# Kernel tuning notes

Measured on AMD Instinct MI355X. Metric: run time of the kernel, lower is better.

## Reference

```python
import jax, jax.numpy as jnp
import numpy as np

D_MODEL = 1024
BLOCK_SIZE = 2048


def setup_inputs() -> dict:
    key = jax.random.key(0)
    ks = jax.random.split(key, 9)
    B, T, C = 4, 2048, D_MODEL
    s = 1.0 / np.sqrt(C)
    return {
        "x": jax.random.normal(ks[0], (B, T, C), dtype=jnp.float32),
        "Wq": jax.random.normal(ks[1], (C, C), dtype=jnp.float32) * s,
        "bq": jnp.zeros((C,), dtype=jnp.float32),
        "Wk": jax.random.normal(ks[2], (C, C), dtype=jnp.float32) * s,
        "bk": jnp.zeros((C,), dtype=jnp.float32),
        "Wv": jax.random.normal(ks[3], (C, C), dtype=jnp.float32) * s,
        "bv": jnp.zeros((C,), dtype=jnp.float32),
        "Wo": jax.random.normal(ks[4], (C, C), dtype=jnp.float32) * s,
        "bo": jnp.zeros((C,), dtype=jnp.float32),
    }


def reference(x, Wq, bq, Wk, bk, Wv, bv, Wo, bo):
    B, T, C = x.shape
    q = x @ Wq + bq
    k = x @ Wk + bk
    v = x @ Wv + bv
    # NOTE: original module never splits heads; attention is over full d_model
    score = jnp.einsum("btc,bsc->bts", q, k) / jnp.sqrt(jnp.asarray(C, x.dtype))
    causal = jnp.tril(jnp.ones((T, T), dtype=bool))
    score = jnp.where(causal, score, jnp.asarray(-jnp.inf, x.dtype))
    probs = jax.nn.softmax(score, axis=-1)
    out = jnp.einsum("bts,bsc->btc", probs, v)
    return out @ Wo + bo
```

## Files before the change

### kernel.cpp

```cpp
#include <hip/hip_runtime.h>
#include <hip/hip_bf16.h>
#include <stdint.h>


typedef __attribute__((ext_vector_type(8))) __bf16 bf16x8;
typedef __attribute__((ext_vector_type(4))) float f32x4;

#define MFMA16(A, B, C) __builtin_amdgcn_mfma_f32_16x16x32_bf16(A, B, C, 0, 0, 0)
#define BAR() asm volatile("s_barrier" ::: "memory")

#define T_SEQ 2048
#define D_MOD 1024

static __device__ __forceinline__ void gload_lds16(const void* g, void* l) {
  __builtin_amdgcn_global_load_lds(
      (const __attribute__((address_space(1))) void*)g,
      (__attribute__((address_space(3))) void*)l, 16, 0, 0);
}

__global__ void cvt_bf16_kernel(const float* __restrict__ in,
                                __bf16* __restrict__ out, int n8) {
  int i = blockIdx.x * blockDim.x + threadIdx.x;
  if (i < n8) {
    const float4* p = (const float4*)(in + (size_t)i * 8);
    float4 a = p[0], b = p[1];
    bf16x8 o;
    o[0] = (__bf16)a.x; o[1] = (__bf16)a.y; o[2] = (__bf16)a.z; o[3] = (__bf16)a.w;
    o[4] = (__bf16)b.x; o[5] = (__bf16)b.y; o[6] = (__bf16)b.z; o[7] = (__bf16)b.w;
    *(bf16x8*)(out + (size_t)i * 8) = o;
  }
}

__global__ void transpose_cvt_kernel(const float* __restrict__ W,
                                     __bf16* __restrict__ Wt) {
  __shared__ float tile[32][33];
  int tx = threadIdx.x, ty = threadIdx.y;
  int bx = blockIdx.x * 32, by = blockIdx.y * 32;
#pragma unroll
  for (int i = 0; i < 4; i++)
    tile[ty + 8 * i][tx] = W[(size_t)(by + ty + 8 * i) * D_MOD + bx + tx];
  __syncthreads();
#pragma unroll
  for (int i = 0; i < 4; i++)
    Wt[(size_t)(bx + ty + 8 * i) * D_MOD + by + tx] = (__bf16)tile[tx][ty + 8 * i];
}

__global__ void transpose_v_kernel(const __bf16* __restrict__ V,
                                   __bf16* __restrict__ Vt) {
  __shared__ __bf16 tile[32][33];
  int tx = threadIdx.x, ty = threadIdx.y;
  int b = blockIdx.z;
  int t0 = blockIdx.x * 32, d0 = blockIdx.y * 32;
  const __bf16* Vb = V + (size_t)b * T_SEQ * D_MOD;
  __bf16* Vtb = Vt + (size_t)b * D_MOD * T_SEQ;
#pragma unroll
  for (int i = 0; i < 4; i++)
    tile[ty + 8 * i][tx] = Vb[(size_t)(t0 + ty + 8 * i) * D_MOD + d0 + tx];
  __syncthreads();
#pragma unroll
  for (int i = 0; i < 4; i++)
    Vtb[(size_t)(d0 + ty + 8 * i) * T_SEQ + t0 + tx] = tile[tx][ty + 8 * i];
}

template <int MG, int NG>
static __device__ __forceinline__ void mfma_quad(f32x4 (&acc)[8][4],
                                                 const bf16x8 (&aR)[4][2],
                                                 const bf16x8 (&bR)[2][2]) {
#pragma unroll
  for (int i = 0; i < 4; i++)
#pragma unroll
    for (int n = 0; n < 2; n++)
#pragma unroll
      for (int kk = 0; kk < 2; kk++)
        acc[MG * 4 + i][NG * 2 + n] =
            MFMA16(aR[i][kk], bR[n][kk], acc[MG * 4 + i][NG * 2 + n]);
}

template <int MODE>
__global__ __launch_bounds__(512, 2) void gemm8_kernel(
    const __bf16* __restrict__ A, const __bf16* __restrict__ Bt,
    const float* __restrict__ b0, const float* __restrict__ b1,
    const float* __restrict__ b2, void* __restrict__ o0,
    void* __restrict__ o1, void* __restrict__ o2, int lda, int ldb,
    size_t bsA, size_t bsB, size_t bsC) {
  constexpr int NT = 16;
  __shared__ __align__(16) char lds[131072];
#define ABUF(p, h) (lds + ((p) * 2 + (h)) * 16384)
#define BBUF(p, h) (lds + 65536 + ((p) * 2 + (h)) * 16384)

  const int tid = threadIdx.x;
  const int w = tid >> 6, l = tid & 63;
  const int wr = w >> 2, wc = w & 3;
  int bm, bn;
  if (MODE == 0) {
    const int cpx = gridDim.x >> 3;
    const int swz = ((int)blockIdx.x & 7) * cpx + ((int)blockIdx.x >> 3);
    bm = (swz / 12) * 256;
    bn = (swz % 12) * 256;
  } else {
    if ((int)blockIdx.y > (int)blockIdx.x) return;
    bm = blockIdx.x * 256;
    bn = blockIdx.y * 256;
  }
  const int z = blockIdx.z;
  A += (size_t)z * bsA;
  Bt += (size_t)z * bsB;

  const int grow = l >> 2;
  const int cswz = (l & 3) ^ ((l >> 3) & 3);
  const int rlo = l & 15;
  const int xsw = (((l >> 4) ^ ((l >> 1) & 3)) << 4);

#define STAGE_A(t, h)                                                        \
  {                                                                          \
    const __bf16* g = A + (size_t)(bm + (h) * 128 + w * 16 + grow) * lda +   \
                      (t) * 64 + cswz * 8;                                   \
    char* d = ABUF((t) & 1, h) + w * 1024 + l * 16;                          \
    gload_lds16(g, d);                                                       \
    gload_lds16(g + 32, d + 8192);                                           \
  }
#define STAGE_B(t, h)                                                        \
  {                                                                          \
    const __bf16* g = Bt + (size_t)(bn + (h) * 128 + w * 16 + grow) * ldb +  \
                      (t) * 64 + cswz * 8;                                   \
    char* d = BBUF((t) & 1, h) + w * 1024 + l * 16;                          \
    gload_lds16(g, d);                                                       \
    gload_lds16(g + 32, d + 8192);                                           \
  }
#define LDA_FRAG(p, g, i, kk)                                     \
  (*(const bf16x8*)(ABUF(p, wr) + (kk) * 8192 +                   \
                    ((g) * 64 + (i) * 16 + rlo) * 64 + xsw))
#define LDB_FRAG(p, g, n, kk)                                     \
  (*(const bf16x8*)(BBUF(p, (wc >> 1)) + (kk) * 8192 +            \
                    ((wc & 1) * 64 + (g) * 32 + (n) * 16 + rlo) * 64 + xsw))

  f32x4 acc[8][4] = {};
  STAGE_A(0, 0); STAGE_A(0, 1);
  STAGE_B(0, 0); STAGE_B(0, 1);
  STAGE_A(1, 0); STAGE_A(1, 1);
  asm volatile("s_waitcnt vmcnt(4)" ::: "memory");
  BAR();

  for (int t = 0; t < NT; ++t) {
    const int p = t & 1;
    bf16x8 a[4][2], b[2][2];
#pragma unroll
    for (int i = 0; i < 4; i++) {
      a[i][0] = LDA_FRAG(p, 0, i, 0);
      a[i][1] = LDA_FRAG(p, 0, i, 1);
    }
#pragma unroll
    for (int n = 0; n < 2; n++) {
      b[n][0] = LDB_FRAG(p, 0, n, 0);
      b[n][1] = LDB_FRAG(p, 0, n, 1);
    }
    if (t + 1 < NT) STAGE_B(t + 1, 0);
    BAR();
    __builtin_amdgcn_s_setprio(1);
    mfma_quad<0, 0>(acc, a, b);
    __builtin_amdgcn_s_setprio(0);
    BAR();
    bf16x8 b2[2][2];
#pragma unroll
    for (int n = 0; n < 2; n++) {
      b2[n][0] = LDB_FRAG(p, 1, n, 0);
      b2[n][1] = LDB_FRAG(p, 1, n, 1);
    }
    if (t + 1 < NT) STAGE_B(t + 1, 1);
    BAR();
    __builtin_amdgcn_s_setprio(1);
    mfma_quad<0, 1>(acc, a, b2);
    __builtin_amdgcn_s_setprio(0);
    BAR();
#pragma unroll
    for (int i = 0; i < 4; i++) {
      a[i][0] = LDA_FRAG(p, 1, i, 0);
      a[i][1] = LDA_FRAG(p, 1, i, 1);
    }
    BAR();
    __builtin_amdgcn_s_setprio(1);
    mfma_quad<1, 1>(acc, a, b2);
    __builtin_amdgcn_s_setprio(0);
    BAR();
#pragma unroll
    for (int n = 0; n < 2; n++) {
      b[n][0] = LDB_FRAG(p, 0, n, 0);
      b[n][1] = LDB_FRAG(p, 0, n, 1);
    }
    if (t + 2 < NT) {
      STAGE_A(t + 2, 0); STAGE_A(t + 2, 1);
      BAR();
      __builtin_amdgcn_s_setprio(1);
      mfma_quad<1, 0>(acc, a, b);
      __builtin_amdgcn_s_setprio(0);
      asm volatile("s_waitcnt vmcnt(4)" ::: "memory");
      BAR();
    } else {
      BAR();
      __builtin_amdgcn_s_setprio(1);
      mfma_quad<1, 0>(acc, a, b);
      __builtin_amdgcn_s_setprio(0);
      asm volatile("s_waitcnt vmcnt(0)" ::: "memory");
      BAR();
    }
  }

  if (MODE == 0) {
    const int seg = bn >> 10;
    const float* bs = (seg == 0) ? b0 : (seg == 1) ? b1 : b2;
    __bf16* os = (__bf16*)((seg == 0) ? o0 : (seg == 1) ? o1 : o2);
    const int bnl = bn & 1023;
#pragma unroll
    for (int n4 = 0; n4 < 4; n4++) {
      int col = bnl + wc * 64 + n4 * 16 + rlo;
      float bvv = bs[col];
#pragma unroll
      for (int mi = 0; mi < 8; mi++) {
        int row = bm + wr * 128 + mi * 16 + (l >> 4) * 4;
#pragma unroll
        for (int r = 0; r < 4; r++)
          os[(size_t)(row + r) * D_MOD + col] = (__bf16)(acc[mi][n4][r] + bvv);
      }
    }
  } else {
    float* os = (float*)o0 + (size_t)z * bsC;
#pragma unroll
    for (int n4 = 0; n4 < 4; n4++) {
      int col = bn + wc * 64 + n4 * 16 + rlo;
#pragma unroll
      for (int mi = 0; mi < 8; mi++) {
        int rowb = bm + wr * 128 + mi * 16 + (l >> 4) * 4;
#pragma unroll
        for (int r = 0; r < 4; r++) {
          int row = rowb + r;
          float v = acc[mi][n4][r] * 0.03125f;
          if (col > row) v = -1e30f;
          os[(size_t)row * T_SEQ + col] = v;
        }
      }
    }
  }
#undef ABUF
#undef BBUF
#undef STAGE_A
#undef STAGE_B
#undef LDA_FRAG
#undef LDB_FRAG
}

template <int MODE>
__global__ __launch_bounds__(512, 2) void ugemm_kernel(
    const __bf16* __restrict__ A, const __bf16* __restrict__ Bt,
    const float* __restrict__ b0, void* __restrict__ o0, int lda, int ldb,
    size_t bsA, size_t bsB, size_t bsC) {
  __shared__ __align__(16) char lds[147456];
#define ABUF(p3) (lds + (p3) * 16384)
#define BBUF(p3) (lds + 49152 + (p3) * 32768)

  const int tid = threadIdx.x;
  const int w = tid >> 6, l = tid & 63;
  const int wr = w >> 2, wc = w & 3;
  const int z = blockIdx.z;

  int bm, bn, NT;
  if (MODE == 1) {
    const int cpx = gridDim.x >> 3;
    const int swz = ((int)blockIdx.x & 7) * cpx + ((int)blockIdx.x >> 3);
    bm = (swz >> 2) * 128; bn = (swz & 3) * 256; NT = 16;
  } else {
    const int i = (int)blockIdx.x >> 2;
    bm = i * 128; bn = ((int)blockIdx.x & 3) * 256; NT = (i + 1) * 2;
  }
  A += (size_t)z * bsA;
  Bt += (size_t)z * bsB;

  const int grow = w * 16 + (l >> 2);
  const int cswz = (l & 3) ^ ((l >> 3) & 3);
  const int rlo = l & 15;
  const int xsw = (((l >> 4) ^ ((l >> 1) & 3)) << 4);

#define STAGE_A(t, p3)                                                       \
  {                                                                          \
    const __bf16* g = A + (size_t)(bm + grow) * lda + (t) * 64 + cswz * 8;   \
    char* d = ABUF(p3) + w * 1024 + l * 16;                                  \
    gload_lds16(g, d);                                                       \
    gload_lds16(g + 32, d + 8192);                                           \
  }
#define STAGE_B(t, p3)                                                       \
  {                                                                          \
    const __bf16* g = Bt + (size_t)(bn + grow) * ldb + (t) * 64 + cswz * 8;  \
    char* d = BBUF(p3) + w * 1024 + l * 16;                                  \
    gload_lds16(g, d);                                                       \
    gload_lds16(g + 32, d + 16384);                                          \
    const __bf16* g2 = g + (size_t)128 * ldb;                                \
    gload_lds16(g2, d + 8192);                                               \
    gload_lds16(g2 + 32, d + 8192 + 16384);                                  \
  }
#define LDA_FRAG(p3, i, kk)                                       \
  (*(const bf16x8*)(ABUF(p3) + (kk) * 8192 +                      \
                    (wr * 64 + (i) * 16 + rlo) * 64 + xsw))
#define LDB_FRAG(p3, n, kk)                                       \
  (*(const bf16x8*)(BBUF(p3) + (kk) * 16384 +                     \
                    (wc * 64 + (n) * 16 + rlo) * 64 + xsw))

  f32x4 acc[4][4] = {};
  STAGE_A(0, 0); STAGE_B(0, 0);
  STAGE_A(1, 1); STAGE_B(1, 1);
  asm volatile("s_waitcnt vmcnt(6)" ::: "memory");
  BAR();

  int p = 0, pn2 = 2;
  for (int t = 0; t < NT; ++t) {
    bf16x8 af[4][2], bf01[2][2], bf23[2][2];
#pragma unroll
    for (int i = 0; i < 4; i++) {
      af[i][0] = LDA_FRAG(p, i, 0);
      af[i][1] = LDA_FRAG(p, i, 1);
    }
#pragma unroll
    for (int n = 0; n < 2; n++) {
      bf01[n][0] = LDB_FRAG(p, n, 0);
      bf01[n][1] = LDB_FRAG(p, n, 1);
    }
    if (t + 2 < NT) STAGE_A(t + 2, pn2);
    BAR();
    __builtin_amdgcn_s_setprio(1);
#pragma unroll
    for (int i = 0; i < 4; i++)
#pragma unroll
      for (int n = 0; n < 2; n++) {
        acc[i][n] = MFMA16(af[i][0], bf01[n][0], acc[i][n]);
        acc[i][n] = MFMA16(af[i][1], bf01[n][1], acc[i][n]);
      }
    __builtin_amdgcn_s_setprio(0);
    BAR();
#pragma unroll
    for (int n = 0; n < 2; n++) {
      bf23[n][0] = LDB_FRAG(p, n + 2, 0);
      bf23[n][1] = LDB_FRAG(p, n + 2, 1);
    }
    if (t + 2 < NT) STAGE_B(t + 2, pn2);
    BAR();
    __builtin_amdgcn_s_setprio(1);
#pragma unroll
    for (int i = 0; i < 4; i++)
#pragma unroll
      for (int n = 0; n < 2; n++) {
        acc[i][n + 2] = MFMA16(af[i][0], bf23[n][0], acc[i][n + 2]);
        acc[i][n + 2] = MFMA16(af[i][1], bf23[n][1], acc[i][n + 2]);
      }
    __builtin_amdgcn_s_setprio(0);
    if (t + 2 < NT) {
      asm volatile("s_waitcnt vmcnt(6)" ::: "memory");
    } else {
      asm volatile("s_waitcnt vmcnt(0)" ::: "memory");
    }
    BAR();
    p = (p + 1 == 3) ? 0 : p + 1;
    pn2 = (pn2 + 1 == 3) ? 0 : pn2 + 1;
  }

  if (MODE == 1) {
    float* os = (float*)o0;
#pragma unroll
    for (int n = 0; n < 4; n++) {
      int col = bn + wc * 64 + n * 16 + rlo;
      float bvv = b0[col];
#pragma unroll
      for (int m = 0; m < 4; m++) {
        int rowb = bm + wr * 64 + m * 16 + (l >> 4) * 4;
#pragma unroll
        for (int r = 0; r < 4; r++)
          os[(size_t)(rowb + r) * D_MOD + col] = acc[m][n][r] + bvv;
      }
    }
  } else {
    __bf16* os = (__bf16*)o0 + (size_t)z * bsC;
#pragma unroll
    for (int n = 0; n < 4; n++) {
      int col = bn + wc * 64 + n * 16 + rlo;
#pragma unroll
      for (int m = 0; m < 4; m++) {
        int rowb = bm + wr * 64 + m * 16 + (l >> 4) * 4;
#pragma unroll
        for (int r = 0; r < 4; r++)
          os[(size_t)(rowb + r) * D_MOD + col] = (__bf16)acc[m][n][r];
      }
    }
  }
#undef ABUF
#undef BBUF
#undef STAGE_A
#undef STAGE_B
#undef LDA_FRAG
#undef LDB_FRAG
}

__global__ __launch_bounds__(256) void softmax_kernel(float* __restrict__ S,
                                                      size_t bstride) {
  const int t = blockIdx.x, b = blockIdx.y;
  float* Srow = S + (size_t)b * bstride + (size_t)t * T_SEQ;
  __bf16* Prow = (__bf16*)Srow;
  const int L = ((t + 1) + 127) & ~127;
  const int tid = threadIdx.x;
  const int base = tid * 8;
  const bool act = base < L;
  float v[8];
  float m = -1e30f;
  if (act) {
    float4 a = *(const float4*)(Srow + base);
    float4 c = *(const float4*)(Srow + base + 4);
    v[0] = a.x; v[1] = a.y; v[2] = a.z; v[3] = a.w;
    v[4] = c.x; v[5] = c.y; v[6] = c.z; v[7] = c.w;
#pragma unroll
    for (int j = 0; j < 8; j++) m = fmaxf(m, v[j]);
  }
#pragma unroll
  for (int off = 1; off < 64; off <<= 1) m = fmaxf(m, __shfl_xor(m, off));
  __shared__ float redm[4], reds[4];
  const int wave = tid >> 6, lane = tid & 63;
  if (lane == 0) redm[wave] = m;
  __syncthreads();
  m = fmaxf(fmaxf(redm[0], redm[1]), fmaxf(redm[2], redm[3]));
  float p[8];
  float s = 0.f;
  if (act) {
#pragma unroll
    for (int j = 0; j < 8; j++) {
      p[j] = __expf(v[j] - m);
      s += p[j];
    }
  }
#pragma unroll
  for (int off = 1; off < 64; off <<= 1) s += __shfl_xor(s, off);
  if (lane == 0) reds[wave] = s;
  __syncthreads();
  const float inv = 1.0f / (reds[0] + reds[1] + reds[2] + reds[3]);
  if (act) {
    bf16x8 o;
#pragma unroll
    for (int j = 0; j < 8; j++) o[j] = (__bf16)(p[j] * inv);
    *(bf16x8*)(Prow + base) = o;
  }
}

extern "C" void kernel_launch(void* const* d_in, const int* in_sizes, int n_in,
                              void* d_out, int out_size, void* d_ws,
                              size_t ws_size, hipStream_t stream) {
  const float* x = (const float*)d_in[0];
  const float* Wq = (const float*)d_in[1];
  const float* bq = (const float*)d_in[2];
  const float* Wk = (const float*)d_in[3];
  const float* bk = (const float*)d_in[4];
  const float* Wv = (const float*)d_in[5];
  const float* bv = (const float*)d_in[6];
  const float* Wo = (const float*)d_in[7];
  const float* bo = (const float*)d_in[8];

  char* ws = (char*)d_ws;
  const size_t MB = 1u << 20;
  const size_t TC = (size_t)T_SEQ * D_MOD;
  const size_t TT = (size_t)T_SEQ * T_SEQ;
  __bf16* xb    = (__bf16*)(ws);
  __bf16* Wqkvt = (__bf16*)(ws + 16 * MB);
  __bf16* Wot   = (__bf16*)(ws + 22 * MB);
  __bf16* Qb    = (__bf16*)(ws + 24 * MB);
  __bf16* Kb    = (__bf16*)(ws + 40 * MB);
  __bf16* Vb    = (__bf16*)(ws + 56 * MB);
  __bf16* Vtb   = (__bf16*)(ws);

  cvt_bf16_kernel<<<4096, 256, 0, stream>>>(x, xb, 8192 * D_MOD / 8);
  dim3 tb(32, 8);
  transpose_cvt_kernel<<<dim3(32, 32), tb, 0, stream>>>(Wq, Wqkvt);
  transpose_cvt_kernel<<<dim3(32, 32), tb, 0, stream>>>(Wk, Wqkvt + 1024 * 1024);
  transpose_cvt_kernel<<<dim3(32, 32), tb, 0, stream>>>(Wv, Wqkvt + 2048 * 1024);
  transpose_cvt_kernel<<<dim3(32, 32), tb, 0, stream>>>(Wo, Wot);
  gemm8_kernel<0><<<384, 512, 0, stream>>>(xb, Wqkvt, bq, bk, bv, Qb, Kb, Vb,
                                           D_MOD, D_MOD, 0, 0, 0);
  transpose_v_kernel<<<dim3(64, 32, 4), tb, 0, stream>>>(Vb, Vtb);

  const bool batched = ws_size >= 137 * MB;
  if (batched) {
    float* S = (float*)(ws + 72 * MB);
    __bf16* AO = Vb;
    gemm8_kernel<3><<<dim3(8, 8, 4), 512, 0, stream>>>(
        Qb, Kb, nullptr, nullptr, nullptr, S, nullptr, nullptr, D_MOD, D_MOD,
        TC, TC, TT);
    softmax_kernel<<<dim3(T_SEQ, 4), 256, 0, stream>>>(S, TT);
    ugemm_kernel<2><<<dim3(64, 1, 4), 512, 0, stream>>>(
        (const __bf16*)S, Vtb, nullptr, AO, 2 * T_SEQ, T_SEQ, TT * 2,
        (size_t)D_MOD * T_SEQ, TC);
    ugemm_kernel<1><<<256, 512, 0, stream>>>(AO, Wot, bo, d_out, D_MOD, D_MOD,
                                             0, 0, 0);
  } else {
    float* S = (float*)(ws + 56 * MB);
    __bf16* AO = Qb;
    for (int b = 0; b < 4; ++b) {
      gemm8_kernel<3><<<dim3(8, 8, 1), 512, 0, stream>>>(
          Qb + b * TC, Kb + b * TC, nullptr, nullptr, nullptr, S, nullptr,
          nullptr, D_MOD, D_MOD, 0, 0, 0);
      softmax_kernel<<<dim3(T_SEQ, 1), 256, 0, stream>>>(S, 0);
      ugemm_kernel<2><<<dim3(64, 1, 1), 512, 0, stream>>>(
          (const __bf16*)S, Vtb + b * TC, nullptr, AO + b * TC, 2 * T_SEQ,
          T_SEQ, 0, 0, 0);
    }
    ugemm_kernel<1><<<256, 512, 0, stream>>>(AO, Wot, bo, d_out, D_MOD, D_MOD,
                                             0, 0, 0);
  }
}
```

Before: 197.4 us.

## Fuse V transpose into QKV epilogue, merge weight transposes, rebalance causal PV tiles

The QKV GEMM epilogue now writes V directly transposed, which removes the separate transpose_v kernel. The four weight transposes become one launch. The 256x256 GEMM mainloop is simplified to a single-buffered 64KB-LDS loop. The PV GEMM uses 128x128 tiles, and each block processes a short and a long causal row block together to balance work. Risks: the single-buffered GEMM may expose load latency, and the transposed V stores are strided 8-byte writes.

```diff
diff --git a/kernel.cpp b/kernel.cpp
--- a/kernel.cpp
+++ b/kernel.cpp
@@ -4,6 +4,7 @@
 
 
 typedef __attribute__((ext_vector_type(8))) __bf16 bf16x8;
+typedef __attribute__((ext_vector_type(4))) __bf16 bf16x4;
 typedef __attribute__((ext_vector_type(4))) float f32x4;
 
 #define MFMA16(A, B, C) __builtin_amdgcn_mfma_f32_16x16x32_bf16(A, B, C, 0, 0, 0)
@@ -31,9 +32,16 @@
   }
 }
 
-__global__ void transpose_cvt_kernel(const float* __restrict__ W,
-                                     __bf16* __restrict__ Wt) {
+__global__ void transpose_cvt4_kernel(const float* __restrict__ Wq,
+                                      const float* __restrict__ Wk,
+                                      const float* __restrict__ Wv,
+                                      const float* __restrict__ Wo,
+                                      __bf16* __restrict__ Wqkvt,
+                                      __bf16* __restrict__ Wot) {
   __shared__ float tile[32][33];
+  const int z = blockIdx.z;
+  const float* W = (z == 0) ? Wq : (z == 1) ? Wk : (z == 2) ? Wv : Wo;
+  __bf16* Wt = (z < 3) ? (Wqkvt + (size_t)z * 1024 * 1024) : Wot;
   int tx = threadIdx.x, ty = threadIdx.y;
   int bx = blockIdx.x * 32, by = blockIdx.y * 32;
 #pragma unroll
@@ -45,48 +53,17 @@
     Wt[(size_t)(bx + ty + 8 * i) * D_MOD + by + tx] = (__bf16)tile[tx][ty + 8 * i];
 }
 
-__global__ void transpose_v_kernel(const __bf16* __restrict__ V,
-                                   __bf16* __restrict__ Vt) {
-  __shared__ __bf16 tile[32][33];
-  int tx = threadIdx.x, ty = threadIdx.y;
-  int b = blockIdx.z;
-  int t0 = blockIdx.x * 32, d0 = blockIdx.y * 32;
-  const __bf16* Vb = V + (size_t)b * T_SEQ * D_MOD;
-  __bf16* Vtb = Vt + (size_t)b * D_MOD * T_SEQ;
-#pragma unroll
-  for (int i = 0; i < 4; i++)
-    tile[ty + 8 * i][tx] = Vb[(size_t)(t0 + ty + 8 * i) * D_MOD + d0 + tx];
-  __syncthreads();
-#pragma unroll
-  for (int i = 0; i < 4; i++)
-    Vtb[(size_t)(d0 + ty + 8 * i) * T_SEQ + t0 + tx] = tile[tx][ty + 8 * i];
-}
-
-template <int MG, int NG>
-static __device__ __forceinline__ void mfma_quad(f32x4 (&acc)[8][4],
-                                                 const bf16x8 (&aR)[4][2],
-                                                 const bf16x8 (&bR)[2][2]) {
-#pragma unroll
-  for (int i = 0; i < 4; i++)
-#pragma unroll
-    for (int n = 0; n < 2; n++)
-#pragma unroll
-      for (int kk = 0; kk < 2; kk++)
-        acc[MG * 4 + i][NG * 2 + n] =
-            MFMA16(aR[i][kk], bR[n][kk], acc[MG * 4 + i][NG * 2 + n]);
-}
-
 template <int MODE>
-__global__ __launch_bounds__(512, 2) void gemm8_kernel(
+__global__ __launch_bounds__(512, 2) void sbg_kernel(
     const __bf16* __restrict__ A, const __bf16* __restrict__ Bt,
-    const float* __restrict__ b0, const float* __restrict__ b1,
-    const float* __restrict__ b2, void* __restrict__ o0,
-    void* __restrict__ o1, void* __restrict__ o2, int lda, int ldb,
-    size_t bsA, size_t bsB, size_t bsC) {
+    const float* __restrict__ bq, const float* __restrict__ bk,
+    const float* __restrict__ bv, void* __restrict__ o0,
+    void* __restrict__ o1, void* __restrict__ o2, size_t bsA, size_t bsB,
+    size_t bsC) {
   constexpr int NT = 16;
-  __shared__ __align__(16) char lds[131072];
-#define ABUF(p, h) (lds + ((p) * 2 + (h)) * 16384)
-#define BBUF(p, h) (lds + 65536 + ((p) * 2 + (h)) * 16384)
+  __shared__ __align__(16) char lds[65536];
+  char* ABUF = lds;
+  char* BBUF = lds + 32768;
 
   const int tid = threadIdx.x;
   const int w = tid >> 6, l = tid & 63;
@@ -103,123 +80,101 @@
     bn = blockIdx.y * 256;
   }
   const int z = blockIdx.z;
-  A += (size_t)z * bsA;
-  Bt += (size_t)z * bsB;
-
-  const int grow = l >> 2;
+  const __bf16* Ag = A + (size_t)z * bsA + (size_t)bm * 1024;
+  const __bf16* Bg = Bt + (size_t)z * bsB + (size_t)bn * 1024;
+
   const int cswz = (l & 3) ^ ((l >> 3) & 3);
   const int rlo = l & 15;
   const int xsw = (((l >> 4) ^ ((l >> 1) & 3)) << 4);
-
-#define STAGE_A(t, h)                                                        \
-  {                                                                          \
-    const __bf16* g = A + (size_t)(bm + (h) * 128 + w * 16 + grow) * lda +   \
-                      (t) * 64 + cswz * 8;                                   \
-    char* d = ABUF((t) & 1, h) + w * 1024 + l * 16;                          \
-    gload_lds16(g, d);                                                       \
-    gload_lds16(g + 32, d + 8192);                                           \
-  }
-#define STAGE_B(t, h)                                                        \
-  {                                                                          \
-    const __bf16* g = Bt + (size_t)(bn + (h) * 128 + w * 16 + grow) * ldb +  \
-                      (t) * 64 + cswz * 8;                                   \
-    char* d = BBUF((t) & 1, h) + w * 1024 + l * 16;                          \
-    gload_lds16(g, d);                                                       \
-    gload_lds16(g + 32, d + 8192);                                           \
-  }
-#define LDA_FRAG(p, g, i, kk)                                     \
-  (*(const bf16x8*)(ABUF(p, wr) + (kk) * 8192 +                   \
-                    ((g) * 64 + (i) * 16 + rlo) * 64 + xsw))
-#define LDB_FRAG(p, g, n, kk)                                     \
-  (*(const bf16x8*)(BBUF(p, (wc >> 1)) + (kk) * 8192 +            \
-                    ((wc & 1) * 64 + (g) * 32 + (n) * 16 + rlo) * 64 + xsw))
+  const int srow = w * 16 + (l >> 2);
+
+#define SSTAGE(dst, gsrc, t)                                              \
+  {                                                                       \
+    _Pragma("unroll") for (int h = 0; h < 2; h++) {                       \
+      const __bf16* g =                                                   \
+          (gsrc) + (size_t)(h * 128 + srow) * 1024 + (t) * 64 + cswz * 8; \
+      char* d = (dst) + h * 8192 + w * 1024 + l * 16;                     \
+      gload_lds16(g, d);                                                  \
+      gload_lds16(g + 32, d + 16384);                                     \
+    }                                                                     \
+  }
 
   f32x4 acc[8][4] = {};
-  STAGE_A(0, 0); STAGE_A(0, 1);
-  STAGE_B(0, 0); STAGE_B(0, 1);
-  STAGE_A(1, 0); STAGE_A(1, 1);
-  asm volatile("s_waitcnt vmcnt(4)" ::: "memory");
+  SSTAGE(ABUF, Ag, 0);
+  SSTAGE(BBUF, Bg, 0);
+  asm volatile("s_waitcnt vmcnt(0)" ::: "memory");
   BAR();
 
   for (int t = 0; t < NT; ++t) {
-    const int p = t & 1;
-    bf16x8 a[4][2], b[2][2];
-#pragma unroll
-    for (int i = 0; i < 4; i++) {
-      a[i][0] = LDA_FRAG(p, 0, i, 0);
-      a[i][1] = LDA_FRAG(p, 0, i, 1);
-    }
-#pragma unroll
-    for (int n = 0; n < 2; n++) {
-      b[n][0] = LDB_FRAG(p, 0, n, 0);
-      b[n][1] = LDB_FRAG(p, 0, n, 1);
-    }
-    if (t + 1 < NT) STAGE_B(t + 1, 0);
-    BAR();
+    bf16x8 af[8][2], bf[4][2];
+#pragma unroll
+    for (int i = 0; i < 8; i++) {
+#pragma unroll
+      for (int kk = 0; kk < 2; kk++)
+        af[i][kk] = *(const bf16x8*)(ABUF + kk * 16384 +
+                                     (wr * 128 + i * 16 + rlo) * 64 + xsw);
+    }
+#pragma unroll
+    for (int n = 0; n < 4; n++) {
+#pragma unroll
+      for (int kk = 0; kk < 2; kk++)
+        bf[n][kk] = *(const bf16x8*)(BBUF + kk * 16384 +
+                                     (wc * 64 + n * 16 + rlo) * 64 + xsw);
+    }
+    asm volatile("s_waitcnt lgkmcnt(0)" ::: "memory");
+    BAR();
+    if (t + 1 < NT) {
+      SSTAGE(ABUF, Ag, t + 1);
+      SSTAGE(BBUF, Bg, t + 1);
+    }
     __builtin_amdgcn_s_setprio(1);
-    mfma_quad<0, 0>(acc, a, b);
+#pragma unroll
+    for (int kk = 0; kk < 2; kk++)
+#pragma unroll
+      for (int i = 0; i < 8; i++)
+#pragma unroll
+        for (int n = 0; n < 4; n++)
+          acc[i][n] = MFMA16(af[i][kk], bf[n][kk], acc[i][n]);
     __builtin_amdgcn_s_setprio(0);
-    BAR();
-    bf16x8 b2[2][2];
-#pragma unroll
-    for (int n = 0; n < 2; n++) {
-      b2[n][0] = LDB_FRAG(p, 1, n, 0);
-      b2[n][1] = LDB_FRAG(p, 1, n, 1);
-    }
-    if (t + 1 < NT) STAGE_B(t + 1, 1);
-    BAR();
-    __builtin_amdgcn_s_setprio(1);
-    mfma_quad<0, 1>(acc, a, b2);
-    __builtin_amdgcn_s_setprio(0);
-    BAR();
-#pragma unroll
-    for (int i = 0; i < 4; i++) {
-      a[i][0] = LDA_FRAG(p, 1, i, 0);
-      a[i][1] = LDA_FRAG(p, 1, i, 1);
-    }
-    BAR();
-    __builtin_amdgcn_s_setprio(1);
-    mfma_quad<1, 1>(acc, a, b2);
-    __builtin_amdgcn_s_setprio(0);
-    BAR();
-#pragma unroll
-    for (int n = 0; n < 2; n++) {
-      b[n][0] = LDB_FRAG(p, 0, n, 0);
-      b[n][1] = LDB_FRAG(p, 0, n, 1);
-    }
-    if (t + 2 < NT) {
-      STAGE_A(t + 2, 0); STAGE_A(t + 2, 1);
-      BAR();
-      __builtin_amdgcn_s_setprio(1);
-      mfma_quad<1, 0>(acc, a, b);
-      __builtin_amdgcn_s_setprio(0);
-      asm volatile("s_waitcnt vmcnt(4)" ::: "memory");
-      BAR();
-    } else {
-      BAR();
-      __builtin_amdgcn_s_setprio(1);
-      mfma_quad<1, 0>(acc, a, b);
-      __builtin_amdgcn_s_setprio(0);
-      asm volatile("s_waitcnt vmcnt(0)" ::: "memory");
-      BAR();
-    }
-  }
-
+    asm volatile("s_waitcnt vmcnt(0)" ::: "memory");
+    BAR();
+  }
+
+  const int l4 = (l >> 4) * 4;
   if (MODE == 0) {
     const int seg = bn >> 10;
-    const float* bs = (seg == 0) ? b0 : (seg == 1) ? b1 : b2;
-    __bf16* os = (__bf16*)((seg == 0) ? o0 : (seg == 1) ? o1 : o2);
     const int bnl = bn & 1023;
-#pragma unroll
-    for (int n4 = 0; n4 < 4; n4++) {
-      int col = bnl + wc * 64 + n4 * 16 + rlo;
-      float bvv = bs[col];
-#pragma unroll
-      for (int mi = 0; mi < 8; mi++) {
-        int row = bm + wr * 128 + mi * 16 + (l >> 4) * 4;
-#pragma unroll
-        for (int r = 0; r < 4; r++)
-          os[(size_t)(row + r) * D_MOD + col] = (__bf16)(acc[mi][n4][r] + bvv);
+    if (seg < 2) {
+      const float* bs = seg ? bk : bq;
+      __bf16* os = (__bf16*)(seg ? o1 : o0);
+#pragma unroll
+      for (int n4 = 0; n4 < 4; n4++) {
+        int col = bnl + wc * 64 + n4 * 16 + rlo;
+        float bvv = bs[col];
+#pragma unroll
+        for (int mi = 0; mi < 8; mi++) {
+          int row = bm + wr * 128 + mi * 16 + l4;
+#pragma unroll
+          for (int r = 0; r < 4; r++)
+            os[(size_t)(row + r) * D_MOD + col] = (__bf16)(acc[mi][n4][r] + bvv);
+        }
+      }
+    } else {
+      __bf16* os = (__bf16*)o2;
+#pragma unroll
+      for (int n4 = 0; n4 < 4; n4++) {
+        int lcol = bnl + wc * 64 + n4 * 16 + rlo;
+        float bvv = bv[lcol];
+#pragma unroll
+        for (int mi = 0; mi < 8; mi++) {
+          int rowb = bm + wr * 128 + mi * 16 + l4;
+          int zz = rowb >> 11, tt = rowb & 2047;
+          bf16x4 pk;
+#pragma unroll
+          for (int r = 0; r < 4; r++) pk[r] = (__bf16)(acc[mi][n4][r] + bvv);
+          *(bf16x4*)(os + (size_t)zz * (D_MOD * T_SEQ) + (size_t)lcol * T_SEQ +
+                     tt) = pk;
+        }
       }
     }
   } else {
@@ -229,7 +184,7 @@
       int col = bn + wc * 64 + n4 * 16 + rlo;
 #pragma unroll
       for (int mi = 0; mi < 8; mi++) {
-        int rowb = bm + wr * 128 + mi * 16 + (l >> 4) * 4;
+        int rowb = bm + wr * 128 + mi * 16 + l4;
 #pragma unroll
         for (int r = 0; r < 4; r++) {
           int row = rowb + r;
@@ -240,59 +195,150 @@
       }
     }
   }
-#undef ABUF
-#undef BBUF
-#undef STAGE_A
-#undef STAGE_B
-#undef LDA_FRAG
-#undef LDB_FRAG
-}
-
-template <int MODE>
-__global__ __launch_bounds__(512, 2) void ugemm_kernel(
-    const __bf16* __restrict__ A, const __bf16* __restrict__ Bt,
-    const float* __restrict__ b0, void* __restrict__ o0, int lda, int ldb,
-    size_t bsA, size_t bsB, size_t bsC) {
-  __shared__ __align__(16) char lds[147456];
+#undef SSTAGE
+}
+
+__global__ __launch_bounds__(512, 2) void pv_kernel(
+    const __bf16* __restrict__ Ap, const __bf16* __restrict__ Btp,
+    __bf16* __restrict__ Op, size_t bsA, size_t bsB, size_t bsC) {
+  __shared__ __align__(16) char lds[98304];
 #define ABUF(p3) (lds + (p3) * 16384)
-#define BBUF(p3) (lds + 49152 + (p3) * 32768)
+#define BBUF(p3) (lds + 49152 + (p3) * 16384)
 
   const int tid = threadIdx.x;
   const int w = tid >> 6, l = tid & 63;
   const int wr = w >> 2, wc = w & 3;
+  const int pid = (int)blockIdx.x >> 3;
+  const int bn = ((int)blockIdx.x & 7) * 128;
   const int z = blockIdx.z;
-
-  int bm, bn, NT;
-  if (MODE == 1) {
-    const int cpx = gridDim.x >> 3;
-    const int swz = ((int)blockIdx.x & 7) * cpx + ((int)blockIdx.x >> 3);
-    bm = (swz >> 2) * 128; bn = (swz & 3) * 256; NT = 16;
-  } else {
-    const int i = (int)blockIdx.x >> 2;
-    bm = i * 128; bn = ((int)blockIdx.x & 3) * 256; NT = (i + 1) * 2;
-  }
-  A += (size_t)z * bsA;
-  Bt += (size_t)z * bsB;
+  const __bf16* A = Ap + (size_t)z * bsA;
+  const __bf16* Bt = Btp + (size_t)z * bsB;
+  __bf16* O = Op + (size_t)z * bsC;
 
   const int grow = w * 16 + (l >> 2);
   const int cswz = (l & 3) ^ ((l >> 3) & 3);
   const int rlo = l & 15;
   const int xsw = (((l >> 4) ^ ((l >> 1) & 3)) << 4);
 
-#define STAGE_A(t, p3)                                                       \
+#define PSTAGE_A(t, p3)                                                      \
   {                                                                          \
-    const __bf16* g = A + (size_t)(bm + grow) * lda + (t) * 64 + cswz * 8;   \
+    const __bf16* g = A + (size_t)(bm + grow) * 4096 + (t) * 64 + cswz * 8;  \
     char* d = ABUF(p3) + w * 1024 + l * 16;                                  \
     gload_lds16(g, d);                                                       \
     gload_lds16(g + 32, d + 8192);                                           \
   }
+#define PSTAGE_B(t, p3)                                                      \
+  {                                                                          \
+    const __bf16* g = Bt + (size_t)(bn + grow) * 2048 + (t) * 64 + cswz * 8; \
+    char* d = BBUF(p3) + w * 1024 + l * 16;                                  \
+    gload_lds16(g, d);                                                       \
+    gload_lds16(g + 32, d + 8192);                                           \
+  }
+#define PLDA(p3, i, kk)                                           \
+  (*(const bf16x8*)(ABUF(p3) + (kk) * 8192 +                      \
+                    (wr * 64 + (i) * 16 + rlo) * 64 + xsw))
+#define PLDB(p3, n, kk)                                           \
+  (*(const bf16x8*)(BBUF(p3) + (kk) * 8192 +                      \
+                    (wc * 32 + (n) * 16 + rlo) * 64 + xsw))
+
+#pragma unroll
+  for (int seg = 0; seg < 2; ++seg) {
+    const int i = seg ? (15 - pid) : pid;
+    const int bm = i * 128;
+    const int NT = (i + 1) * 2;
+    f32x4 acc[4][2] = {};
+
+    PSTAGE_A(0, 0); PSTAGE_B(0, 0);
+    if (NT > 1) { PSTAGE_A(1, 1); PSTAGE_B(1, 1); }
+    asm volatile("s_waitcnt vmcnt(4)" ::: "memory");
+    BAR();
+
+    int p = 0, pn2 = 2;
+    for (int t = 0; t < NT; ++t) {
+      bf16x8 af[4][2], bfv[2][2];
+#pragma unroll
+      for (int m = 0; m < 4; m++) {
+        af[m][0] = PLDA(p, m, 0);
+        af[m][1] = PLDA(p, m, 1);
+      }
+#pragma unroll
+      for (int n = 0; n < 2; n++) {
+        bfv[n][0] = PLDB(p, n, 0);
+        bfv[n][1] = PLDB(p, n, 1);
+      }
+      if (t + 2 < NT) { PSTAGE_A(t + 2, pn2); PSTAGE_B(t + 2, pn2); }
+      BAR();
+      __builtin_amdgcn_s_setprio(1);
+#pragma unroll
+      for (int m = 0; m < 4; m++)
+#pragma unroll
+        for (int n = 0; n < 2; n++) {
+          acc[m][n] = MFMA16(af[m][0], bfv[n][0], acc[m][n]);
+          acc[m][n] = MFMA16(af[m][1], bfv[n][1], acc[m][n]);
+        }
+      __builtin_amdgcn_s_setprio(0);
+      if (t + 2 < NT) asm volatile("s_waitcnt vmcnt(4)" ::: "memory");
+      else asm volatile("s_waitcnt vmcnt(0)" ::: "memory");
+      BAR();
+      p = (p + 1 == 3) ? 0 : p + 1;
+      pn2 = (pn2 + 1 == 3) ? 0 : pn2 + 1;
+    }
+
+#pragma unroll
+    for (int n = 0; n < 2; n++) {
+      int col = bn + wc * 32 + n * 16 + rlo;
+#pragma unroll
+      for (int m = 0; m < 4; m++) {
+        int rowb = bm + wr * 64 + m * 16 + (l >> 4) * 4;
+#pragma unroll
+        for (int r = 0; r < 4; r++)
+          O[(size_t)(rowb + r) * D_MOD + col] = (__bf16)acc[m][n][r];
+      }
+    }
+    BAR();
+  }
+#undef ABUF
+#undef BBUF
+#undef PSTAGE_A
+#undef PSTAGE_B
+#undef PLDA
+#undef PLDB
+}
+
+__global__ __launch_bounds__(512, 2) void oproj_kernel(
+    const __bf16* __restrict__ A, const __bf16* __restrict__ Bt,
+    const float* __restrict__ b0, float* __restrict__ o0) {
+  constexpr int NT = 16;
+  __shared__ __align__(16) char lds[147456];
+#define ABUF(p3) (lds + (p3) * 16384)
+#define BBUF(p3) (lds + 49152 + (p3) * 32768)
+
+  const int tid = threadIdx.x;
+  const int w = tid >> 6, l = tid & 63;
+  const int wr = w >> 2, wc = w & 3;
+  const int cpx = gridDim.x >> 3;
+  const int swz = ((int)blockIdx.x & 7) * cpx + ((int)blockIdx.x >> 3);
+  const int bm = (swz >> 2) * 128, bn = (swz & 3) * 256;
+
+  const int grow = w * 16 + (l >> 2);
+  const int cswz = (l & 3) ^ ((l >> 3) & 3);
+  const int rlo = l & 15;
+  const int xsw = (((l >> 4) ^ ((l >> 1) & 3)) << 4);
+
+#define STAGE_A(t, p3)                                                       \
+  {                                                                          \
+    const __bf16* g = A + (size_t)(bm + grow) * 1024 + (t) * 64 + cswz * 8;  \
+    char* d = ABUF(p3) + w * 1024 + l * 16;                                  \
+    gload_lds16(g, d);                                                       \
+    gload_lds16(g + 32, d + 8192);                                           \
+  }
 #define STAGE_B(t, p3)                                                       \
   {                                                                          \
-    const __bf16* g = Bt + (size_t)(bn + grow) * ldb + (t) * 64 + cswz * 8;  \
+    const __bf16* g = Bt + (size_t)(bn + grow) * 1024 + (t) * 64 + cswz * 8; \
     char* d = BBUF(p3) + w * 1024 + l * 16;                                  \
     gload_lds16(g, d);                                                       \
     gload_lds16(g + 32, d + 16384);                                          \
-    const __bf16* g2 = g + (size_t)128 * ldb;                                \
+    const __bf16* g2 = g + (size_t)128 * 1024;                               \
     gload_lds16(g2, d + 8192);                                               \
     gload_lds16(g2 + 32, d + 8192 + 16384);                                  \
   }
@@ -360,32 +406,16 @@
     pn2 = (pn2 + 1 == 3) ? 0 : pn2 + 1;
   }
 
-  if (MODE == 1) {
-    float* os = (float*)o0;
-#pragma unroll
-    for (int n = 0; n < 4; n++) {
-      int col = bn + wc * 64 + n * 16 + rlo;
-      float bvv = b0[col];
-#pragma unroll
-      for (int m = 0; m < 4; m++) {
-        int rowb = bm + wr * 64 + m * 16 + (l >> 4) * 4;
-#pragma unroll
-        for (int r = 0; r < 4; r++)
-          os[(size_t)(rowb + r) * D_MOD + col] = acc[m][n][r] + bvv;
-      }
-    }
-  } else {
-    __bf16* os = (__bf16*)o0 + (size_t)z * bsC;
-#pragma unroll
-    for (int n = 0; n < 4; n++) {
-      int col = bn + wc * 64 + n * 16 + rlo;
-#pragma unroll
-      for (int m = 0; m < 4; m++) {
-        int rowb = bm + wr * 64 + m * 16 + (l >> 4) * 4;
-#pragma unroll
-        for (int r = 0; r < 4; r++)
-          os[(size_t)(rowb + r) * D_MOD + col] = (__bf16)acc[m][n][r];
-      }
+#pragma unroll
+  for (int n = 0; n < 4; n++) {
+    int col = bn + wc * 64 + n * 16 + rlo;
+    float bvv = b0[col];
+#pragma unroll
+    for (int m = 0; m < 4; m++) {
+      int rowb = bm + wr * 64 + m * 16 + (l >> 4) * 4;
+#pragma unroll
+      for (int r = 0; r < 4; r++)
+        o0[(size_t)(rowb + r) * D_MOD + col] = acc[m][n][r] + bvv;
     }
   }
 #undef ABUF
@@ -466,45 +496,35 @@
   __bf16* Wot   = (__bf16*)(ws + 22 * MB);
   __bf16* Qb    = (__bf16*)(ws + 24 * MB);
   __bf16* Kb    = (__bf16*)(ws + 40 * MB);
-  __bf16* Vb    = (__bf16*)(ws + 56 * MB);
-  __bf16* Vtb   = (__bf16*)(ws);
+  __bf16* Vtb   = (__bf16*)(ws + 56 * MB);
 
   cvt_bf16_kernel<<<4096, 256, 0, stream>>>(x, xb, 8192 * D_MOD / 8);
-  dim3 tb(32, 8);
-  transpose_cvt_kernel<<<dim3(32, 32), tb, 0, stream>>>(Wq, Wqkvt);
-  transpose_cvt_kernel<<<dim3(32, 32), tb, 0, stream>>>(Wk, Wqkvt + 1024 * 1024);
-  transpose_cvt_kernel<<<dim3(32, 32), tb, 0, stream>>>(Wv, Wqkvt + 2048 * 1024);
-  transpose_cvt_kernel<<<dim3(32, 32), tb, 0, stream>>>(Wo, Wot);
-  gemm8_kernel<0><<<384, 512, 0, stream>>>(xb, Wqkvt, bq, bk, bv, Qb, Kb, Vb,
-                                           D_MOD, D_MOD, 0, 0, 0);
-  transpose_v_kernel<<<dim3(64, 32, 4), tb, 0, stream>>>(Vb, Vtb);
+  transpose_cvt4_kernel<<<dim3(32, 32, 4), dim3(32, 8), 0, stream>>>(
+      Wq, Wk, Wv, Wo, Wqkvt, Wot);
+  sbg_kernel<0><<<384, 512, 0, stream>>>(xb, Wqkvt, bq, bk, bv, Qb, Kb, Vtb,
+                                         0, 0, 0);
 
   const bool batched = ws_size >= 137 * MB;
   if (batched) {
     float* S = (float*)(ws + 72 * MB);
-    __bf16* AO = Vb;
-    gemm8_kernel<3><<<dim3(8, 8, 4), 512, 0, stream>>>(
-        Qb, Kb, nullptr, nullptr, nullptr, S, nullptr, nullptr, D_MOD, D_MOD,
-        TC, TC, TT);
+    __bf16* AO = Qb;
+    sbg_kernel<3><<<dim3(8, 8, 4), 512, 0, stream>>>(
+        Qb, Kb, nullptr, nullptr, nullptr, S, nullptr, nullptr, TC, TC, TT);
     softmax_kernel<<<dim3(T_SEQ, 4), 256, 0, stream>>>(S, TT);
-    ugemm_kernel<2><<<dim3(64, 1, 4), 512, 0, stream>>>(
-        (const __bf16*)S, Vtb, nullptr, AO, 2 * T_SEQ, T_SEQ, TT * 2,
-        (size_t)D_MOD * T_SEQ, TC);
-    ugemm_kernel<1><<<256, 512, 0, stream>>>(AO, Wot, bo, d_out, D_MOD, D_MOD,
-                                             0, 0, 0);
+    pv_kernel<<<dim3(64, 1, 4), 512, 0, stream>>>((const __bf16*)S, Vtb, AO,
+                                                  TT * 2, TC, TC);
+    oproj_kernel<<<256, 512, 0, stream>>>(AO, Wot, bo, (float*)d_out);
   } else {
-    float* S = (float*)(ws + 56 * MB);
+    float* S = (float*)(ws);
     __bf16* AO = Qb;
     for (int b = 0; b < 4; ++b) {
-      gemm8_kernel<3><<<dim3(8, 8, 1), 512, 0, stream>>>(
+      sbg_kernel<3><<<dim3(8, 8, 1), 512, 0, stream>>>(
           Qb + b * TC, Kb + b * TC, nullptr, nullptr, nullptr, S, nullptr,
-          nullptr, D_MOD, D_MOD, 0, 0, 0);
+          nullptr, 0, 0, 0);
       softmax_kernel<<<dim3(T_SEQ, 1), 256, 0, stream>>>(S, 0);
-      ugemm_kernel<2><<<dim3(64, 1, 1), 512, 0, stream>>>(
-          (const __bf16*)S, Vtb + b * TC, nullptr, AO + b * TC, 2 * T_SEQ,
-          T_SEQ, 0, 0, 0);
-    }
-    ugemm_kernel<1><<<256, 512, 0, stream>>>(AO, Wot, bo, d_out, D_MOD, D_MOD,
-                                             0, 0, 0);
-  }
-}
+      pv_kernel<<<dim3(64, 1, 1), 512, 0, stream>>>(
+          (const __bf16*)S, Vtb + b * TC, AO + b * TC, 0, 0, 0);
+    }
+    oproj_kernel<<<256, 512, 0, stream>>>(AO, Wot, bo, (float*)d_out);
+  }
+}
```

Measured after the change: 189.0 us. 1.04x faster.
